# Kernel optimization log

Hardware: AMD Instinct MI355X
Metric: run time of the kernel (lower is better)

The kernel has to match this reference:

```python
import jax, jax.numpy as jnp
import numpy as np


def setup_inputs() -> dict:
    key = jax.random.key(0)
    num_views = 8
    bs = 4096
    c = 2048
    vision_features = jax.random.normal(key, (num_views * bs, c), dtype=jnp.float32)
    return {"vision_features": vision_features, "num_views": num_views}


def reference(vision_features, num_views):
    # vision_features: [num_views * bs, c]
    n, c = vision_features.shape
    # reshape to (num_views, bs, c) then permute to (bs, num_views, c)
    f = vision_features.reshape(num_views, -1, c).transpose(1, 0, 2)
    # L2-normalize each view feature along channel dim
    f = f / jnp.linalg.norm(f, axis=2, keepdims=True)
    # batched cosine similarity matrix: [bs, V, V]
    sim = jnp.einsum('bvc,bwc->bvw', f, f)
    # strict upper-triangular (off-diagonal) entries, same order as torch.triu_indices
    rows, cols = jnp.triu_indices(num_views, k=1)
    vals = sim[:, rows, cols]  # [bs, P] with P = V*(V-1)/2
    # torch.var default is unbiased (ddof=1)
    var = jnp.var(vals, axis=1, ddof=1)
    return -var
```

## Files before the change

kernel.cpp:

```cpp
#include <hip/hip_runtime.h>
#include <hip/hip_bf16.h>

#define NV   8
#define BSZ  4096
#define CCH  2048
#define NPAIR 28
#define NACC  36
#define BLK  256

__device__ __forceinline__ constexpr int triIdx(int v, int w) {
    return v * NV - (v * (v - 1)) / 2 + (w - v);
}

__global__ __launch_bounds__(BLK) void interviews_kernel(
        const float* __restrict__ in, float* __restrict__ out) {
    const int b = blockIdx.x;
    const int t = threadIdx.x;

    float acc[NACC];
#pragma unroll
    for (int i = 0; i < NACC; ++i) acc[i] = 0.0f;

    const float* base = in + (size_t)b * CCH;

#pragma unroll
    for (int j = 0; j < CCH / (BLK * 4); ++j) {
        float4 x[NV];
#pragma unroll
        for (int v = 0; v < NV; ++v) {
            const float* p = base + (size_t)v * BSZ * CCH + (size_t)j * BLK * 4 + (size_t)t * 4;
            x[v] = *reinterpret_cast<const float4*>(p);
        }
        int idx = 0;
#pragma unroll
        for (int v = 0; v < NV; ++v) {
#pragma unroll
            for (int w = v; w < NV; ++w) {
                acc[idx] += x[v].x * x[w].x + x[v].y * x[w].y
                          + x[v].z * x[w].z + x[v].w * x[w].w;
                ++idx;
            }
        }
    }

#pragma unroll
    for (int i = 0; i < NACC; ++i) {
        float v = acc[i];
#pragma unroll
        for (int off = 32; off > 0; off >>= 1)
            v += __shfl_down(v, off, 64);
        acc[i] = v;
    }

    __shared__ float red[BLK / 64][NACC];
    const int wave = t >> 6;
    const int lane = t & 63;
    if (lane == 0) {
#pragma unroll
        for (int i = 0; i < NACC; ++i) red[wave][i] = acc[i];
    }
    __syncthreads();

    if (t == 0) {
        float G[NACC];
#pragma unroll
        for (int i = 0; i < NACC; ++i)
            G[i] = red[0][i] + red[1][i] + red[2][i] + red[3][i];

        float rn[NV];
#pragma unroll
        for (int v = 0; v < NV; ++v)
            rn[v] = 1.0f / sqrtf(G[triIdx(v, v)]);

        float s[NPAIR];
        float mean = 0.0f;
        int k = 0;
#pragma unroll
        for (int v = 0; v < NV; ++v) {
#pragma unroll
            for (int w = v + 1; w < NV; ++w) {
                s[k] = G[triIdx(v, w)] * rn[v] * rn[w];
                mean += s[k];
                ++k;
            }
        }
        mean *= (1.0f / NPAIR);

        float var = 0.0f;
#pragma unroll
        for (int i = 0; i < NPAIR; ++i) {
            float d = s[i] - mean;
            var += d * d;
        }
        var *= (1.0f / (NPAIR - 1));

        out[b] = -var;
    }
}

extern "C" void kernel_launch(void* const* d_in, const int* in_sizes, int n_in,
                              void* d_out, int out_size, void* d_ws, size_t ws_size,
                              hipStream_t stream) {
    const float* in = (const float*)d_in[0];
    float* out = (float*)d_out;
    interviews_kernel<<<dim3(out_size), dim3(BLK), 0, stream>>>(in, out);
}
```

Before: 54.14 us.

## Map one wavefront per batch row and drop shared-memory block reduction

Each 64-lane wavefront now handles one batch element, looping over 8 chunks of channels, so the block covers four rows and the grid shrinks by four. The LDS reduction and __syncthreads are replaced by an xor-shuffle reduction within the wave. Loads use nontemporal hints and the launch bounds request higher occupancy. The cost is more serial work and register pressure per lane (36 accumulators plus 8 vector loads), with a possible drop in memory-level parallelism per wave.

```diff
diff --git a/kernel.cpp b/kernel.cpp
--- a/kernel.cpp
+++ b/kernel.cpp
@@ -1,43 +1,48 @@
 #include <hip/hip_runtime.h>
 #include <hip/hip_bf16.h>
 
-#define NV   8
-#define BSZ  4096
-#define CCH  2048
+#define NV    8
+#define BSZ   4096
+#define CCH   2048
 #define NPAIR 28
 #define NACC  36
-#define BLK  256
+#define BLK   256
+#define VSTR  ((size_t)BSZ * CCH)
+
+typedef float f32x4 __attribute__((ext_vector_type(4)));
 
 __device__ __forceinline__ constexpr int triIdx(int v, int w) {
     return v * NV - (v * (v - 1)) / 2 + (w - v);
 }
 
-__global__ __launch_bounds__(BLK) void interviews_kernel(
+__global__ __launch_bounds__(BLK, 4) void interviews_kernel(
         const float* __restrict__ in, float* __restrict__ out) {
-    const int b = blockIdx.x;
-    const int t = threadIdx.x;
+    const int lane = threadIdx.x & 63;
+    const int wv   = threadIdx.x >> 6;
+    const int b    = blockIdx.x * (BLK / 64) + wv;
 
     float acc[NACC];
 #pragma unroll
     for (int i = 0; i < NACC; ++i) acc[i] = 0.0f;
 
-    const float* base = in + (size_t)b * CCH;
+    const float* base = in + (size_t)b * CCH + (size_t)lane * 4;
 
-#pragma unroll
-    for (int j = 0; j < CCH / (BLK * 4); ++j) {
-        float4 x[NV];
+#pragma unroll 2
+    for (int j = 0; j < CCH / (64 * 4); ++j) {
+        f32x4 x[NV];
 #pragma unroll
         for (int v = 0; v < NV; ++v) {
-            const float* p = base + (size_t)v * BSZ * CCH + (size_t)j * BLK * 4 + (size_t)t * 4;
-            x[v] = *reinterpret_cast<const float4*>(p);
+            const f32x4* p = reinterpret_cast<const f32x4*>(
+                base + (size_t)v * VSTR + (size_t)j * 256);
+            x[v] = __builtin_nontemporal_load(p);
         }
         int idx = 0;
 #pragma unroll
         for (int v = 0; v < NV; ++v) {
 #pragma unroll
             for (int w = v; w < NV; ++w) {
-                acc[idx] += x[v].x * x[w].x + x[v].y * x[w].y
-                          + x[v].z * x[w].z + x[v].w * x[w].w;
+                acc[idx] += x[v][0] * x[w][0] + x[v][1] * x[w][1]
+                          + x[v][2] * x[w][2] + x[v][3] * x[w][3];
                 ++idx;
             }
         }
@@ -47,30 +52,16 @@
     for (int i = 0; i < NACC; ++i) {
         float v = acc[i];
 #pragma unroll
-        for (int off = 32; off > 0; off >>= 1)
-            v += __shfl_down(v, off, 64);
+        for (int off = 1; off < 64; off <<= 1)
+            v += __shfl_xor(v, off, 64);
         acc[i] = v;
     }
 
-    __shared__ float red[BLK / 64][NACC];
-    const int wave = t >> 6;
-    const int lane = t & 63;
     if (lane == 0) {
-#pragma unroll
-        for (int i = 0; i < NACC; ++i) red[wave][i] = acc[i];
-    }
-    __syncthreads();
-
-    if (t == 0) {
-        float G[NACC];
-#pragma unroll
-        for (int i = 0; i < NACC; ++i)
-            G[i] = red[0][i] + red[1][i] + red[2][i] + red[3][i];
-
         float rn[NV];
 #pragma unroll
         for (int v = 0; v < NV; ++v)
-            rn[v] = 1.0f / sqrtf(G[triIdx(v, v)]);
+            rn[v] = 1.0f / sqrtf(acc[triIdx(v, v)]);
 
         float s[NPAIR];
         float mean = 0.0f;
@@ -79,7 +70,7 @@
         for (int v = 0; v < NV; ++v) {
 #pragma unroll
             for (int w = v + 1; w < NV; ++w) {
-                s[k] = G[triIdx(v, w)] * rn[v] * rn[w];
+                s[k] = acc[triIdx(v, w)] * rn[v] * rn[w];
                 mean += s[k];
                 ++k;
             }
@@ -103,5 +94,5 @@
                               hipStream_t stream) {
     const float* in = (const float*)d_in[0];
     float* out = (float*)d_out;
-    interviews_kernel<<<dim3(out_size), dim3(BLK), 0, stream>>>(in, out);
+    interviews_kernel<<<dim3(out_size / (BLK / 64)), dim3(BLK), 0, stream>>>(in, out);
 }
```

Measured after the change: 60.11 us. 11.0% more time.
